# Optimization experiments

Hardware: AMD Instinct MI355X
Metric: run time of the kernel (lower is better)

The kernel has to match this reference:

```python
import jax, jax.numpy as jnp
import numpy as np

NUM_BINS = 16
D_MODEL = 128
TAIL_BOUND = 20.0
MIN_BIN_WIDTH = 1e-3
MIN_BIN_HEIGHT = 1e-3
MIN_DERIVATIVE = 1e-3
EPS = 1e-6


def setup_inputs() -> dict:
    key = jax.random.key(0)
    ks = jax.random.split(key, 10)
    B, S = 32, 8192
    sc = 0.05  # small init scale so spline logits stay moderate
    return {
        "inputs": jax.random.normal(ks[0], (B, S), dtype=jnp.float32),
        "conditioning": jax.random.normal(ks[1], (B, S, D_MODEL), dtype=jnp.float32),
        "Ww": jax.random.normal(ks[2], (NUM_BINS, D_MODEL), dtype=jnp.float32) * sc,
        "bw": jax.random.normal(ks[3], (NUM_BINS,), dtype=jnp.float32) * sc,
        "Wh": jax.random.normal(ks[4], (NUM_BINS, D_MODEL), dtype=jnp.float32) * sc,
        "bh": jax.random.normal(ks[5], (NUM_BINS,), dtype=jnp.float32) * sc,
        "Wd": jax.random.normal(ks[6], (NUM_BINS - 1, D_MODEL), dtype=jnp.float32) * sc,
        "bd": jax.random.normal(ks[7], (NUM_BINS - 1,), dtype=jnp.float32) * sc,
        "Wl": jax.random.normal(ks[8], (NUM_BINS, D_MODEL), dtype=jnp.float32) * sc,
        "bl": jax.random.normal(ks[9], (NUM_BINS,), dtype=jnp.float32) * sc,
    }


def _rational_linear_spline(x, uw, uh, ud, ul, left, right, bottom, top):
    nb = uw.shape[-1]
    # bin widths / cumulative widths
    w = MIN_BIN_WIDTH + (1.0 - MIN_BIN_WIDTH * nb) * jax.nn.softmax(uw, axis=-1)
    cw = jnp.concatenate([jnp.zeros_like(w[..., :1]), jnp.cumsum(w, axis=-1)], axis=-1)
    cw = (right - left) * cw + left
    cw = cw.at[..., 0].set(left).at[..., -1].set(right)
    w = cw[..., 1:] - cw[..., :-1]
    # derivatives (ud already padded to nb+1 by caller)
    d = MIN_DERIVATIVE + jax.nn.softplus(ud)
    # bin heights / cumulative heights
    h = MIN_BIN_HEIGHT + (1.0 - MIN_BIN_HEIGHT * nb) * jax.nn.softmax(uh, axis=-1)
    ch = jnp.concatenate([jnp.zeros_like(h[..., :1]), jnp.cumsum(h, axis=-1)], axis=-1)
    ch = (top - bottom) * ch + bottom
    ch = ch.at[..., 0].set(bottom).at[..., -1].set(top)
    h = ch[..., 1:] - ch[..., :-1]
    # searchsorted via sum of comparisons (as in source)
    locs = cw.at[..., -1].add(EPS)
    idx = jnp.sum((x[..., None] >= locs).astype(jnp.int32), axis=-1) - 1
    idx = jnp.clip(idx, 0, nb - 1)
    g = lambda t: jnp.take_along_axis(t, idx[..., None], axis=-1)[..., 0]
    in_cw = g(cw)
    in_bw = g(w)
    in_ch = g(ch)
    in_delta = g(h / w)
    dk = g(d)
    dk1 = g(d[..., 1:])
    in_h = g(h)
    lambdas = 0.95 * jax.nn.sigmoid(ul) + 0.025
    lam = g(lambdas)
    wa = 1.0
    wb = jnp.sqrt(dk / dk1) * wa
    wc = (lam * wa * dk + (1.0 - lam) * wb * dk1) / in_delta
    ya = in_ch
    yb = in_h + in_ch
    yc = ((1.0 - lam) * wa * ya + lam * wb * yb) / ((1.0 - lam) * wa + lam * wb)
    theta = (x - in_cw) / in_bw
    m = theta <= lam
    num = jnp.where(m, wa * ya * (lam - theta) + wc * yc * theta,
                    wc * yc * (1.0 - theta) + wb * yb * (theta - lam))
    den = jnp.where(m, wa * (lam - theta) + wc * theta,
                    wc * (1.0 - theta) + wb * (theta - lam))
    out = num / den
    deriv_num = jnp.where(m, wa * wc * lam * (yc - ya), wb * wc * (1.0 - lam) * (yb - yc)) / in_bw
    logabsdet = jnp.log(deriv_num) - 2.0 * jnp.log(jnp.abs(den))
    return out, logabsdet


def reference(inputs, conditioning, Ww, bw, Wh, bh, Wd, bd, Wl, bl):
    # parameter nets (module.forward): note the module normalizes here AND the
    # spline normalizes again -- replicate faithfully.
    uw = jax.nn.softmax(jnp.einsum('bsd,kd->bsk', conditioning, Ww) + bw, axis=-1)
    uh = jax.nn.softmax(jnp.einsum('bsd,kd->bsk', conditioning, Wh) + bh, axis=-1)
    ud = jax.nn.softplus(jnp.einsum('bsd,kd->bsk', conditioning, Wd) + bd)
    ul = jax.nn.sigmoid(jnp.einsum('bsd,kd->bsk', conditioning, Wl) + bl)
    # linear tails: pad derivatives with constant so boundary derivative == 1
    const = float(np.log(np.exp(1.0 - MIN_DERIVATIVE) - 1.0))
    edge = jnp.full(ud.shape[:-1] + (1,), const, dtype=ud.dtype)
    udp = jnp.concatenate([edge, ud, edge], axis=-1)  # [B,S,nb+1]
    tb = TAIL_BOUND
    inside = (inputs >= -tb) & (inputs <= tb)
    xc = jnp.clip(inputs, -tb, tb)
    s_out, s_lad = _rational_linear_spline(xc, uw, uh, udp, ul, -tb, tb, -tb, tb)
    outputs = jnp.where(inside, s_out, inputs)
    logabsdet = jnp.where(inside, s_lad, 0.0)
    return outputs, logabsdet
```

## Files before the change

### kernel.cpp

```cpp
#include <hip/hip_runtime.h>
#include <math.h>

#define NB 16
#define DM 128
#define BM 256
#define ZSTRIDE 68

typedef _Float16 half8  __attribute__((ext_vector_type(8)));
typedef _Float16 half4v __attribute__((ext_vector_type(4)));
typedef _Float16 half2v __attribute__((ext_vector_type(2)));
typedef __fp16   fp16x2 __attribute__((ext_vector_type(2)));
typedef float    f32x4  __attribute__((ext_vector_type(4)));

__device__ __forceinline__ float frcp_(float x) { return __builtin_amdgcn_rcpf(x); }
__device__ __forceinline__ float softplus_fast(float x) {
    return fmaxf(x, 0.0f) + __logf(1.0f + __expf(-fabsf(x)));
}
__device__ __forceinline__ float sigmoid_fast(float x) {
    return frcp_(1.0f + __expf(-x));
}
__device__ __forceinline__ void softmax16_m(float* z) {
    float m = z[0];
#pragma unroll
    for (int k = 1; k < NB; k++) m = fmaxf(m, z[k]);
    float s = 0.0f;
#pragma unroll
    for (int k = 0; k < NB; k++) { z[k] = __expf(z[k] - m); s += z[k]; }
    float r = frcp_(s);
#pragma unroll
    for (int k = 0; k < NB; k++) z[k] *= r;
}
__device__ __forceinline__ void softmax16_nm(float* z) {
    float s = 0.0f;
#pragma unroll
    for (int k = 0; k < NB; k++) { z[k] = __expf(z[k]); s += z[k]; }
    float r = frcp_(s);
#pragma unroll
    for (int k = 0; k < NB; k++) z[k] *= r;
}

__device__ __forceinline__ half2v pk_(float lo, float hi) {
    fp16x2 p = __builtin_amdgcn_cvt_pkrtz(lo, hi);
    return __builtin_bit_cast(half2v, p);
}
__device__ __forceinline__ half8 cvt8(float4 a0, float4 a1) {
    half2v p0 = pk_(a0.x, a0.y);
    half2v p1 = pk_(a0.z, a0.w);
    half2v p2 = pk_(a1.x, a1.y);
    half2v p3 = pk_(a1.z, a1.w);
    half8 f;
    f[0] = p0[0]; f[1] = p0[1]; f[2] = p1[0]; f[3] = p1[1];
    f[4] = p2[0]; f[5] = p2[1]; f[6] = p3[0]; f[7] = p3[1];
    return f;
}

#define LOADC(c)                                        \
    A##c##_0 = *(const float4*)(cr##c + 0);             \
    A##c##_1 = *(const float4*)(cr##c + 4);             \
    A##c##_2 = *(const float4*)(cr##c + 32);            \
    A##c##_3 = *(const float4*)(cr##c + 36);            \
    A##c##_4 = *(const float4*)(cr##c + 64);            \
    A##c##_5 = *(const float4*)(cr##c + 68);            \
    A##c##_6 = *(const float4*)(cr##c + 96);            \
    A##c##_7 = *(const float4*)(cr##c + 100);

#define CVTC(c)                                         \
    af0 = cvt8(A##c##_0, A##c##_1);                     \
    af1 = cvt8(A##c##_2, A##c##_3);                     \
    af2 = cvt8(A##c##_4, A##c##_5);                     \
    af3 = cvt8(A##c##_6, A##c##_7);

#define MFMA_S(af, s)                                                           \
    acc0 = __builtin_amdgcn_mfma_f32_16x16x32_f16(af, B0##s, acc0, 0, 0, 0);    \
    acc1 = __builtin_amdgcn_mfma_f32_16x16x32_f16(af, B1##s, acc1, 0, 0, 0);    \
    acc2 = __builtin_amdgcn_mfma_f32_16x16x32_f16(af, B2##s, acc2, 0, 0, 0);    \
    acc3 = __builtin_amdgcn_mfma_f32_16x16x32_f16(af, B3##s, acc3, 0, 0, 0);

#define STOREZ(c) {                                                             \
    _Float16* zpw = zbase + (size_t)((c) * 16) * ZSTRIDE;                       \
    _Pragma("unroll")                                                           \
    for (int r = 0; r < 4; r++) {                                               \
        half2v p0 = pk_(acc0[r], acc1[r]);                                      \
        half2v p1 = pk_(acc2[r], acc3[r]);                                      \
        half4v w; w[0] = p0[0]; w[1] = p0[1]; w[2] = p1[0]; w[3] = p1[1];       \
        *(half4v*)(zpw + (size_t)r * ZSTRIDE) = w;                              \
    } }

#define RESET_ACC  acc0 = zf4; acc1 = zf4; acc2 = zf4; acc3 = zf4;

#define STAGE_B(Wt, isWd, Q0, Q1, Q2, Q3) {                                     \
    const bool val = (!(isWd)) || (l15 < 15);                                   \
    const float* srcl = (Wt) + (size_t)(val ? l15 : 0) * DM + lg * 8;           \
    float4 q0 = *(const float4*)(srcl + 0),  q1 = *(const float4*)(srcl + 4);   \
    float4 q2 = *(const float4*)(srcl + 32), q3 = *(const float4*)(srcl + 36);  \
    float4 q4 = *(const float4*)(srcl + 64), q5 = *(const float4*)(srcl + 68);  \
    float4 q6 = *(const float4*)(srcl + 96), q7 = *(const float4*)(srcl + 100); \
    Q0 = val ? cvt8(q0, q1) : hz;                                               \
    Q1 = val ? cvt8(q2, q3) : hz;                                               \
    Q2 = val ? cvt8(q4, q5) : hz;                                               \
    Q3 = val ? cvt8(q6, q7) : hz; }

__global__ __launch_bounds__(256, 2) void spline_mfma(
    const float* __restrict__ xin, const float* __restrict__ cond,
    const float* __restrict__ Ww, const float* __restrict__ bw,
    const float* __restrict__ Wh, const float* __restrict__ bh,
    const float* __restrict__ Wd, const float* __restrict__ bd,
    const float* __restrict__ Wl, const float* __restrict__ bl,
    float* __restrict__ out, float* __restrict__ lad, int N)
{
    __shared__ __align__(16) _Float16 Z[BM * ZSTRIDE];

    const int tid  = threadIdx.x;
    const int wave = tid >> 6;
    const int lane = tid & 63;
    const int l15  = lane & 15;
    const int lg   = lane >> 4;
    const size_t blockRow = (size_t)blockIdx.x * BM;
    const size_t gi = blockRow + tid;

    half8 hz;
    hz[0]=hz[1]=hz[2]=hz[3]=hz[4]=hz[5]=hz[6]=hz[7] = (_Float16)0.0f;
    half8 B00, B01, B02, B03, B10, B11, B12, B13,
          B20, B21, B22, B23, B30, B31, B32, B33;
    STAGE_B(Ww, false, B00, B01, B02, B03)
    STAGE_B(Wh, false, B10, B11, B12, B13)
    STAGE_B(Wl, false, B20, B21, B22, B23)
    STAGE_B(Wd, true,  B30, B31, B32, B33)

    size_t gr0 = blockRow + (size_t)(wave * 64 + l15);
    size_t gr1 = gr0 + 16, gr2 = gr0 + 32, gr3 = gr0 + 48;
    if (gr0 >= (size_t)N) gr0 = (size_t)N - 1;
    if (gr1 >= (size_t)N) gr1 = (size_t)N - 1;
    if (gr2 >= (size_t)N) gr2 = (size_t)N - 1;
    if (gr3 >= (size_t)N) gr3 = (size_t)N - 1;
    const float* cr0 = cond + gr0 * DM + lg * 8;
    const float* cr1 = cond + gr1 * DM + lg * 8;
    const float* cr2 = cond + gr2 * DM + lg * 8;
    const float* cr3 = cond + gr3 * DM + lg * 8;

    float4 A0_0, A0_1, A0_2, A0_3, A0_4, A0_5, A0_6, A0_7;
    float4 A1_0, A1_1, A1_2, A1_3, A1_4, A1_5, A1_6, A1_7;
    float4 A2_0, A2_1, A2_2, A2_3, A2_4, A2_5, A2_6, A2_7;
    float4 A3_0, A3_1, A3_2, A3_3, A3_4, A3_5, A3_6, A3_7;
    LOADC(0)
    LOADC(1)
    LOADC(2)
    LOADC(3)
    float x = xin[gi < (size_t)N ? gi : 0];

    const f32x4 zf4 = {0.f, 0.f, 0.f, 0.f};
    f32x4 acc0 = zf4, acc1 = zf4, acc2 = zf4, acc3 = zf4;
    half8 af0, af1, af2, af3;
    _Float16* zbase = &Z[(size_t)(wave * 64 + lg * 4) * ZSTRIDE + l15 * 4];

    CVTC(0)
    MFMA_S(af0, 0) MFMA_S(af1, 1) MFMA_S(af2, 2) MFMA_S(af3, 3)
    STOREZ(0) RESET_ACC
    CVTC(1)
    MFMA_S(af0, 0) MFMA_S(af1, 1) MFMA_S(af2, 2) MFMA_S(af3, 3)
    STOREZ(1) RESET_ACC
    CVTC(2)
    MFMA_S(af0, 0) MFMA_S(af1, 1) MFMA_S(af2, 2) MFMA_S(af3, 3)
    STOREZ(2) RESET_ACC
    CVTC(3)
    MFMA_S(af0, 0) MFMA_S(af1, 1) MFMA_S(af2, 2) MFMA_S(af3, 3)
    STOREZ(3)

    __builtin_amdgcn_sched_barrier(0);
    asm volatile("s_waitcnt lgkmcnt(0)" ::: "memory");
    __builtin_amdgcn_sched_barrier(0);

    if (gi >= (size_t)N) return;

    float zw[NB], zh[NB], zl[NB], zd[NB - 1];
    const half4v* zr4 = (const half4v*)&Z[(size_t)tid * ZSTRIDE];
#pragma unroll
    for (int j = 0; j < NB; j++) {
        half4v v = zr4[j];
        zw[j] = (float)v[0] + bw[j];
        zh[j] = (float)v[1] + bh[j];
        zl[j] = (float)v[2] + bl[j];
        if (j < NB - 1) zd[j] = (float)v[3] + bd[j];
    }

    float xc = fminf(fmaxf(x, -20.0f), 20.0f);

    softmax16_m(zw);
    softmax16_nm(zw);
    const float scale = (1.0f - 1e-3f * NB);
    float cw[NB + 1];
    cw[0] = -20.0f;
    float cum = 0.0f;
#pragma unroll
    for (int k = 0; k < NB; k++) {
        cum += 1e-3f + scale * zw[k];
        cw[k + 1] = 40.0f * cum - 20.0f;
    }
    cw[NB] = 20.0f;

    softmax16_m(zh);
    softmax16_nm(zh);
    float ch[NB + 1];
    ch[0] = -20.0f;
    cum = 0.0f;
#pragma unroll
    for (int k = 0; k < NB; k++) {
        cum += 1e-3f + scale * zh[k];
        ch[k + 1] = 40.0f * cum - 20.0f;
    }
    ch[NB] = 20.0f;

    float in_cw = cw[0], cw_hi = cw[1], in_ch = ch[0], ch_hi = ch[1];
    float zl_sel = zl[0], zd_lo = zd[0], zd_hi = zd[0];
#pragma unroll
    for (int k = 1; k < NB; k++) {
        bool take = (xc >= cw[k]);
        in_cw  = take ? cw[k]     : in_cw;
        cw_hi  = take ? cw[k + 1] : cw_hi;
        in_ch  = take ? ch[k]     : in_ch;
        ch_hi  = take ? ch[k + 1] : ch_hi;
        zl_sel = take ? zl[k]     : zl_sel;
        zd_lo  = take ? zd[k - 1] : zd_lo;
        zd_hi  = take ? zd[(k < NB - 1) ? k : NB - 2] : zd_hi;
    }
    bool firstbin = (xc <  cw[1]);
    bool lastbin  = (xc >= cw[NB - 1]);

    float in_bw = cw_hi - in_cw;
    float in_h  = ch_hi - in_ch;

    float dk  = firstbin ? 1.0f : (1e-3f + softplus_fast(softplus_fast(zd_lo)));
    float dk1 = lastbin  ? 1.0f : (1e-3f + softplus_fast(softplus_fast(zd_hi)));

    float ul  = sigmoid_fast(zl_sel);
    float lam = 0.95f * sigmoid_fast(ul) + 0.025f;

    float rbw = frcp_(in_bw);
    float in_delta = in_h * rbw;
    float wb = sqrtf(dk * frcp_(dk1));
    float wc = (lam * dk + (1.0f - lam) * wb * dk1) * frcp_(in_delta);
    float ya = in_ch;
    float yb = in_h + in_ch;
    float yc = ((1.0f - lam) * ya + lam * wb * yb) * frcp_((1.0f - lam) + lam * wb);
    float theta = (xc - in_cw) * rbw;
    bool mlt = (theta <= lam);

    float num = mlt ? (ya * (lam - theta) + wc * yc * theta)
                    : (wc * yc * (1.0f - theta) + wb * yb * (theta - lam));
    float den = mlt ? ((lam - theta) + wc * theta)
                    : (wc * (1.0f - theta) + wb * (theta - lam));
    float sout = num * frcp_(den);
    float dnum = (mlt ? (wc * lam * (yc - ya))
                      : (wb * wc * (1.0f - lam) * (yb - yc))) * rbw;
    float slad = __logf(dnum) - 2.0f * __logf(fabsf(den));

    bool inside = (x >= -20.0f) && (x <= 20.0f);
    out[gi] = inside ? sout : x;
    lad[gi] = inside ? slad : 0.0f;
}

extern "C" void kernel_launch(void* const* d_in, const int* in_sizes, int n_in,
                              void* d_out, int out_size, void* d_ws, size_t ws_size,
                              hipStream_t stream) {
    const float* xin  = (const float*)d_in[0];
    const float* cond = (const float*)d_in[1];
    const float* Ww   = (const float*)d_in[2];
    const float* bwp  = (const float*)d_in[3];
    const float* Wh   = (const float*)d_in[4];
    const float* bhp  = (const float*)d_in[5];
    const float* Wd   = (const float*)d_in[6];
    const float* bdp  = (const float*)d_in[7];
    const float* Wl   = (const float*)d_in[8];
    const float* blp  = (const float*)d_in[9];
    int N = in_sizes[0];
    float* out = (float*)d_out;
    float* lad = out + N;
    int grid = (N + BM - 1) / BM;
    hipLaunchKernelGGL(spline_mfma, dim3(grid), dim3(256), 0, stream,
                       xin, cond, Ww, bwp, Wh, bhp, Wd, bdp, Wl, blp, out, lad, N);
}
```

Before: 39.08 us.

## Process two tiles per block, prefetching second tile's conditioning during first epilogue

Each block now handles two 256-row tiles, with the grid halved. Half of the second tile's conditioning loads are issued before the first tile's spline epilogue, so memory latency overlaps with the transcendental math, and the weight fragments are staged once per two tiles. The K-index mapping of lanes also changes: each lane now reads float4s strided by 16 instead of contiguous pairs, applied consistently to A and B. The cost is more register pressure and fewer blocks in flight.

```diff
diff --git a/kernel.cpp b/kernel.cpp
--- a/kernel.cpp
+++ b/kernel.cpp
@@ -54,21 +54,21 @@
     return f;
 }
 
-#define LOADC(c)                                        \
-    A##c##_0 = *(const float4*)(cr##c + 0);             \
-    A##c##_1 = *(const float4*)(cr##c + 4);             \
-    A##c##_2 = *(const float4*)(cr##c + 32);            \
-    A##c##_3 = *(const float4*)(cr##c + 36);            \
-    A##c##_4 = *(const float4*)(cr##c + 64);            \
-    A##c##_5 = *(const float4*)(cr##c + 68);            \
-    A##c##_6 = *(const float4*)(cr##c + 96);            \
-    A##c##_7 = *(const float4*)(cr##c + 100);
-
-#define CVTC(c)                                         \
-    af0 = cvt8(A##c##_0, A##c##_1);                     \
-    af1 = cvt8(A##c##_2, A##c##_3);                     \
-    af2 = cvt8(A##c##_4, A##c##_5);                     \
-    af3 = cvt8(A##c##_6, A##c##_7);
+#define LOADC(P, cr)                                    \
+    P##0 = *(const float4*)((cr) + 0);                  \
+    P##1 = *(const float4*)((cr) + 16);                 \
+    P##2 = *(const float4*)((cr) + 32);                 \
+    P##3 = *(const float4*)((cr) + 48);                 \
+    P##4 = *(const float4*)((cr) + 64);                 \
+    P##5 = *(const float4*)((cr) + 80);                 \
+    P##6 = *(const float4*)((cr) + 96);                 \
+    P##7 = *(const float4*)((cr) + 112);
+
+#define CVTC(P)                                         \
+    af0 = cvt8(P##0, P##1);                             \
+    af1 = cvt8(P##2, P##3);                             \
+    af2 = cvt8(P##4, P##5);                             \
+    af3 = cvt8(P##6, P##7);
 
 #define MFMA_S(af, s)                                                           \
     acc0 = __builtin_amdgcn_mfma_f32_16x16x32_f16(af, B0##s, acc0, 0, 0, 0);    \
@@ -88,17 +88,106 @@
 
 #define RESET_ACC  acc0 = zf4; acc1 = zf4; acc2 = zf4; acc3 = zf4;
 
+#define GEMM_CHUNK(P, c)                                                        \
+    CVTC(P)                                                                     \
+    MFMA_S(af0, 0) MFMA_S(af1, 1) MFMA_S(af2, 2) MFMA_S(af3, 3)                 \
+    STOREZ(c) RESET_ACC
+
 #define STAGE_B(Wt, isWd, Q0, Q1, Q2, Q3) {                                     \
     const bool val = (!(isWd)) || (l15 < 15);                                   \
-    const float* srcl = (Wt) + (size_t)(val ? l15 : 0) * DM + lg * 8;           \
-    float4 q0 = *(const float4*)(srcl + 0),  q1 = *(const float4*)(srcl + 4);   \
-    float4 q2 = *(const float4*)(srcl + 32), q3 = *(const float4*)(srcl + 36);  \
-    float4 q4 = *(const float4*)(srcl + 64), q5 = *(const float4*)(srcl + 68);  \
-    float4 q6 = *(const float4*)(srcl + 96), q7 = *(const float4*)(srcl + 100); \
+    const float* srcl = (Wt) + (size_t)(val ? l15 : 0) * DM + lg * 4;           \
+    float4 q0 = *(const float4*)(srcl + 0),  q1 = *(const float4*)(srcl + 16);  \
+    float4 q2 = *(const float4*)(srcl + 32), q3 = *(const float4*)(srcl + 48);  \
+    float4 q4 = *(const float4*)(srcl + 64), q5 = *(const float4*)(srcl + 80);  \
+    float4 q6 = *(const float4*)(srcl + 96), q7 = *(const float4*)(srcl + 112); \
     Q0 = val ? cvt8(q0, q1) : hz;                                               \
     Q1 = val ? cvt8(q2, q3) : hz;                                               \
     Q2 = val ? cvt8(q4, q5) : hz;                                               \
     Q3 = val ? cvt8(q6, q7) : hz; }
+
+#define FENCE_LDS                                       \
+    __builtin_amdgcn_sched_barrier(0);                  \
+    asm volatile("s_waitcnt lgkmcnt(0)" ::: "memory");  \
+    __builtin_amdgcn_sched_barrier(0);
+
+#define EPILOGUE(xv, giv)                                                        \
+  if ((giv) < (size_t)N) {                                                       \
+    float zw[NB], zh[NB], zl[NB], zd[NB - 1];                                    \
+    const half4v* zr4 = (const half4v*)&Z[(size_t)tid * ZSTRIDE];                \
+    _Pragma("unroll")                                                            \
+    for (int j = 0; j < NB; j++) {                                               \
+        half4v v = zr4[j];                                                       \
+        zw[j] = (float)v[0] + bw[j];                                             \
+        zh[j] = (float)v[1] + bh[j];                                             \
+        zl[j] = (float)v[2] + bl[j];                                             \
+        if (j < NB - 1) zd[j] = (float)v[3] + bd[j];                             \
+    }                                                                            \
+    float xc = fminf(fmaxf((xv), -20.0f), 20.0f);                                \
+    softmax16_m(zw);                                                             \
+    softmax16_nm(zw);                                                            \
+    const float scale = (1.0f - 1e-3f * NB);                                     \
+    float cw[NB + 1];                                                            \
+    cw[0] = -20.0f;                                                              \
+    float cum = 0.0f;                                                            \
+    _Pragma("unroll")                                                            \
+    for (int k = 0; k < NB; k++) {                                               \
+        cum += 1e-3f + scale * zw[k];                                            \
+        cw[k + 1] = 40.0f * cum - 20.0f;                                         \
+    }                                                                            \
+    cw[NB] = 20.0f;                                                              \
+    softmax16_m(zh);                                                             \
+    softmax16_nm(zh);                                                            \
+    float ch[NB + 1];                                                            \
+    ch[0] = -20.0f;                                                              \
+    cum = 0.0f;                                                                  \
+    _Pragma("unroll")                                                            \
+    for (int k = 0; k < NB; k++) {                                               \
+        cum += 1e-3f + scale * zh[k];                                            \
+        ch[k + 1] = 40.0f * cum - 20.0f;                                         \
+    }                                                                            \
+    ch[NB] = 20.0f;                                                              \
+    float in_cw = cw[0], cw_hi = cw[1], in_ch = ch[0], ch_hi = ch[1];            \
+    float zl_sel = zl[0], zd_lo = zd[0], zd_hi = zd[0];                          \
+    _Pragma("unroll")                                                            \
+    for (int k = 1; k < NB; k++) {                                               \
+        bool take = (xc >= cw[k]);                                               \
+        in_cw  = take ? cw[k]     : in_cw;                                       \
+        cw_hi  = take ? cw[k + 1] : cw_hi;                                       \
+        in_ch  = take ? ch[k]     : in_ch;                                       \
+        ch_hi  = take ? ch[k + 1] : ch_hi;                                       \
+        zl_sel = take ? zl[k]     : zl_sel;                                      \
+        zd_lo  = take ? zd[k - 1] : zd_lo;                                       \
+        zd_hi  = take ? zd[(k < NB - 1) ? k : NB - 2] : zd_hi;                   \
+    }                                                                            \
+    bool firstbin = (xc <  cw[1]);                                               \
+    bool lastbin  = (xc >= cw[NB - 1]);                                          \
+    float in_bw = cw_hi - in_cw;                                                 \
+    float in_h  = ch_hi - in_ch;                                                 \
+    float dk  = firstbin ? 1.0f : (1e-3f + softplus_fast(softplus_fast(zd_lo))); \
+    float dk1 = lastbin  ? 1.0f : (1e-3f + softplus_fast(softplus_fast(zd_hi))); \
+    float ul  = sigmoid_fast(zl_sel);                                            \
+    float lam = 0.95f * sigmoid_fast(ul) + 0.025f;                               \
+    float rbw = frcp_(in_bw);                                                    \
+    float in_delta = in_h * rbw;                                                 \
+    float wb = sqrtf(dk * frcp_(dk1));                                           \
+    float wc = (lam * dk + (1.0f - lam) * wb * dk1) * frcp_(in_delta);           \
+    float ya = in_ch;                                                            \
+    float yb = in_h + in_ch;                                                     \
+    float yc = ((1.0f - lam) * ya + lam * wb * yb) * frcp_((1.0f - lam) + lam * wb); \
+    float theta = (xc - in_cw) * rbw;                                            \
+    bool mlt = (theta <= lam);                                                   \
+    float num = mlt ? (ya * (lam - theta) + wc * yc * theta)                     \
+                    : (wc * yc * (1.0f - theta) + wb * yb * (theta - lam));      \
+    float den = mlt ? ((lam - theta) + wc * theta)                               \
+                    : (wc * (1.0f - theta) + wb * (theta - lam));                \
+    float sout = num * frcp_(den);                                               \
+    float dnum = (mlt ? (wc * lam * (yc - ya))                                   \
+                      : (wb * wc * (1.0f - lam) * (yb - yc))) * rbw;             \
+    float slad = __logf(dnum) - 2.0f * __logf(fabsf(den));                       \
+    bool inside = ((xv) >= -20.0f) && ((xv) <= 20.0f);                           \
+    out[(giv)] = inside ? sout : (xv);                                           \
+    lad[(giv)] = inside ? slad : 0.0f;                                           \
+  }
 
 __global__ __launch_bounds__(256, 2) void spline_mfma(
     const float* __restrict__ xin, const float* __restrict__ cond,
@@ -115,8 +204,11 @@
     const int lane = tid & 63;
     const int l15  = lane & 15;
     const int lg   = lane >> 4;
-    const size_t blockRow = (size_t)blockIdx.x * BM;
-    const size_t gi = blockRow + tid;
+
+    const int nTiles = (N + BM - 1) / BM;
+    const int t0 = (int)blockIdx.x;
+    const int t1 = t0 + (int)gridDim.x;
+    const bool hasT1 = (t1 < nTiles);
 
     half8 hz;
     hz[0]=hz[1]=hz[2]=hz[3]=hz[4]=hz[5]=hz[6]=hz[7] = (_Float16)0.0f;
@@ -127,136 +219,63 @@
     STAGE_B(Wl, false, B20, B21, B22, B23)
     STAGE_B(Wd, true,  B30, B31, B32, B33)
 
-    size_t gr0 = blockRow + (size_t)(wave * 64 + l15);
-    size_t gr1 = gr0 + 16, gr2 = gr0 + 32, gr3 = gr0 + 48;
-    if (gr0 >= (size_t)N) gr0 = (size_t)N - 1;
-    if (gr1 >= (size_t)N) gr1 = (size_t)N - 1;
-    if (gr2 >= (size_t)N) gr2 = (size_t)N - 1;
-    if (gr3 >= (size_t)N) gr3 = (size_t)N - 1;
-    const float* cr0 = cond + gr0 * DM + lg * 8;
-    const float* cr1 = cond + gr1 * DM + lg * 8;
-    const float* cr2 = cond + gr2 * DM + lg * 8;
-    const float* cr3 = cond + gr3 * DM + lg * 8;
+    const size_t bRow0 = (size_t)t0 * BM;
+    const size_t gi0 = bRow0 + tid;
+    size_t g00 = bRow0 + (size_t)(wave * 64 + l15);
+    size_t g01 = g00 + 16, g02 = g00 + 32, g03 = g00 + 48;
+    if (g00 >= (size_t)N) g00 = (size_t)N - 1;
+    if (g01 >= (size_t)N) g01 = (size_t)N - 1;
+    if (g02 >= (size_t)N) g02 = (size_t)N - 1;
+    if (g03 >= (size_t)N) g03 = (size_t)N - 1;
 
     float4 A0_0, A0_1, A0_2, A0_3, A0_4, A0_5, A0_6, A0_7;
     float4 A1_0, A1_1, A1_2, A1_3, A1_4, A1_5, A1_6, A1_7;
     float4 A2_0, A2_1, A2_2, A2_3, A2_4, A2_5, A2_6, A2_7;
     float4 A3_0, A3_1, A3_2, A3_3, A3_4, A3_5, A3_6, A3_7;
-    LOADC(0)
-    LOADC(1)
-    LOADC(2)
-    LOADC(3)
-    float x = xin[gi < (size_t)N ? gi : 0];
+    LOADC(A0_, cond + g00 * DM + lg * 4)
+    LOADC(A1_, cond + g01 * DM + lg * 4)
+    LOADC(A2_, cond + g02 * DM + lg * 4)
+    LOADC(A3_, cond + g03 * DM + lg * 4)
+    float x0 = xin[gi0 < (size_t)N ? gi0 : 0];
 
     const f32x4 zf4 = {0.f, 0.f, 0.f, 0.f};
     f32x4 acc0 = zf4, acc1 = zf4, acc2 = zf4, acc3 = zf4;
     half8 af0, af1, af2, af3;
     _Float16* zbase = &Z[(size_t)(wave * 64 + lg * 4) * ZSTRIDE + l15 * 4];
 
-    CVTC(0)
-    MFMA_S(af0, 0) MFMA_S(af1, 1) MFMA_S(af2, 2) MFMA_S(af3, 3)
-    STOREZ(0) RESET_ACC
-    CVTC(1)
-    MFMA_S(af0, 0) MFMA_S(af1, 1) MFMA_S(af2, 2) MFMA_S(af3, 3)
-    STOREZ(1) RESET_ACC
-    CVTC(2)
-    MFMA_S(af0, 0) MFMA_S(af1, 1) MFMA_S(af2, 2) MFMA_S(af3, 3)
-    STOREZ(2) RESET_ACC
-    CVTC(3)
-    MFMA_S(af0, 0) MFMA_S(af1, 1) MFMA_S(af2, 2) MFMA_S(af3, 3)
-    STOREZ(3)
-
-    __builtin_amdgcn_sched_barrier(0);
-    asm volatile("s_waitcnt lgkmcnt(0)" ::: "memory");
-    __builtin_amdgcn_sched_barrier(0);
-
-    if (gi >= (size_t)N) return;
-
-    float zw[NB], zh[NB], zl[NB], zd[NB - 1];
-    const half4v* zr4 = (const half4v*)&Z[(size_t)tid * ZSTRIDE];
-#pragma unroll
-    for (int j = 0; j < NB; j++) {
-        half4v v = zr4[j];
-        zw[j] = (float)v[0] + bw[j];
-        zh[j] = (float)v[1] + bh[j];
-        zl[j] = (float)v[2] + bl[j];
-        if (j < NB - 1) zd[j] = (float)v[3] + bd[j];
+    GEMM_CHUNK(A0_, 0)
+    GEMM_CHUNK(A1_, 1)
+    GEMM_CHUNK(A2_, 2)
+    GEMM_CHUNK(A3_, 3)
+
+    const size_t bRow1 = (size_t)t1 * BM;
+    const size_t gi1 = bRow1 + tid;
+    size_t g10 = bRow1 + (size_t)(wave * 64 + l15);
+    size_t g11 = g10 + 16, g12 = g10 + 32, g13 = g10 + 48;
+    if (g10 >= (size_t)N) g10 = (size_t)N - 1;
+    if (g11 >= (size_t)N) g11 = (size_t)N - 1;
+    if (g12 >= (size_t)N) g12 = (size_t)N - 1;
+    if (g13 >= (size_t)N) g13 = (size_t)N - 1;
+    float x1 = 0.0f;
+    if (hasT1) {
+        LOADC(A0_, cond + g10 * DM + lg * 4)
+        LOADC(A1_, cond + g11 * DM + lg * 4)
+        x1 = xin[gi1 < (size_t)N ? gi1 : 0];
     }
 
-    float xc = fminf(fmaxf(x, -20.0f), 20.0f);
-
-    softmax16_m(zw);
-    softmax16_nm(zw);
-    const float scale = (1.0f - 1e-3f * NB);
-    float cw[NB + 1];
-    cw[0] = -20.0f;
-    float cum = 0.0f;
-#pragma unroll
-    for (int k = 0; k < NB; k++) {
-        cum += 1e-3f + scale * zw[k];
-        cw[k + 1] = 40.0f * cum - 20.0f;
+    FENCE_LDS
+    EPILOGUE(x0, gi0)
+
+    if (hasT1) {
+        LOADC(A2_, cond + g12 * DM + lg * 4)
+        LOADC(A3_, cond + g13 * DM + lg * 4)
+        GEMM_CHUNK(A0_, 0)
+        GEMM_CHUNK(A1_, 1)
+        GEMM_CHUNK(A2_, 2)
+        GEMM_CHUNK(A3_, 3)
+        FENCE_LDS
+        EPILOGUE(x1, gi1)
     }
-    cw[NB] = 20.0f;
-
-    softmax16_m(zh);
-    softmax16_nm(zh);
-    float ch[NB + 1];
-    ch[0] = -20.0f;
-    cum = 0.0f;
-#pragma unroll
-    for (int k = 0; k < NB; k++) {
-        cum += 1e-3f + scale * zh[k];
-        ch[k + 1] = 40.0f * cum - 20.0f;
-    }
-    ch[NB] = 20.0f;
-
-    float in_cw = cw[0], cw_hi = cw[1], in_ch = ch[0], ch_hi = ch[1];
-    float zl_sel = zl[0], zd_lo = zd[0], zd_hi = zd[0];
-#pragma unroll
-    for (int k = 1; k < NB; k++) {
-        bool take = (xc >= cw[k]);
-        in_cw  = take ? cw[k]     : in_cw;
-        cw_hi  = take ? cw[k + 1] : cw_hi;
-        in_ch  = take ? ch[k]     : in_ch;
-        ch_hi  = take ? ch[k + 1] : ch_hi;
-        zl_sel = take ? zl[k]     : zl_sel;
-        zd_lo  = take ? zd[k - 1] : zd_lo;
-        zd_hi  = take ? zd[(k < NB - 1) ? k : NB - 2] : zd_hi;
-    }
-    bool firstbin = (xc <  cw[1]);
-    bool lastbin  = (xc >= cw[NB - 1]);
-
-    float in_bw = cw_hi - in_cw;
-    float in_h  = ch_hi - in_ch;
-
-    float dk  = firstbin ? 1.0f : (1e-3f + softplus_fast(softplus_fast(zd_lo)));
-    float dk1 = lastbin  ? 1.0f : (1e-3f + softplus_fast(softplus_fast(zd_hi)));
-
-    float ul  = sigmoid_fast(zl_sel);
-    float lam = 0.95f * sigmoid_fast(ul) + 0.025f;
-
-    float rbw = frcp_(in_bw);
-    float in_delta = in_h * rbw;
-    float wb = sqrtf(dk * frcp_(dk1));
-    float wc = (lam * dk + (1.0f - lam) * wb * dk1) * frcp_(in_delta);
-    float ya = in_ch;
-    float yb = in_h + in_ch;
-    float yc = ((1.0f - lam) * ya + lam * wb * yb) * frcp_((1.0f - lam) + lam * wb);
-    float theta = (xc - in_cw) * rbw;
-    bool mlt = (theta <= lam);
-
-    float num = mlt ? (ya * (lam - theta) + wc * yc * theta)
-                    : (wc * yc * (1.0f - theta) + wb * yb * (theta - lam));
-    float den = mlt ? ((lam - theta) + wc * theta)
-                    : (wc * (1.0f - theta) + wb * (theta - lam));
-    float sout = num * frcp_(den);
-    float dnum = (mlt ? (wc * lam * (yc - ya))
-                      : (wb * wc * (1.0f - lam) * (yb - yc))) * rbw;
-    float slad = __logf(dnum) - 2.0f * __logf(fabsf(den));
-
-    bool inside = (x >= -20.0f) && (x <= 20.0f);
-    out[gi] = inside ? sout : x;
-    lad[gi] = inside ? slad : 0.0f;
 }
 
 extern "C" void kernel_launch(void* const* d_in, const int* in_sizes, int n_in,
@@ -275,7 +294,8 @@
     int N = in_sizes[0];
     float* out = (float*)d_out;
     float* lad = out + N;
-    int grid = (N + BM - 1) / BM;
+    int nTiles = (N + BM - 1) / BM;
+    int grid = (nTiles + 1) / 2;
     hipLaunchKernelGGL(spline_mfma, dim3(grid), dim3(256), 0, stream,
                        xin, cond, Ww, bwp, Wh, bhp, Wd, bdp, Wl, blp, out, lad, N);
 }
```

Result: faster. 35.29 us (-9.7%).
